# Kernel optimization log

Hardware: AMD Instinct MI355X
Metric: run time of the kernel (lower is better)

## Reference

```python
import jax
import jax.numpy as jnp
import numpy as np

B, S, I, H, O = 64, 2048, 128, 128, 128


def setup_inputs() -> dict:
    key = jax.random.key(0)
    ks = jax.random.split(key, 6)
    scale_i = 1.0 / np.sqrt(I)
    scale_h = 1.0 / np.sqrt(H)
    return {
        "x": jax.random.normal(ks[0], (B, S, I), dtype=jnp.float32),
        "Wi": jax.random.normal(ks[1], (I, H), dtype=jnp.float32) * scale_i,
        "Wh": jax.random.normal(ks[2], (H, H), dtype=jnp.float32) * scale_h,
        "b": jax.random.normal(ks[3], (H,), dtype=jnp.float32) * 0.01,
        "Wo": jax.random.normal(ks[4], (H, O), dtype=jnp.float32) * scale_h,
        "bo": jax.random.normal(ks[5], (O,), dtype=jnp.float32) * 0.01,
    }


def reference(x, Wi, Wh, b, Wo, bo):
    # x: [B, S, I]. Recurrence: h_t = relu(tanh(x_t @ Wi + h_{t-1} @ Wh + b))
    # (flax nnx.RNNCell applies tanh inside; the module applies relu on the carry.)
    h0 = jnp.zeros((x.shape[0], Wh.shape[0]), dtype=x.dtype)
    # Pre-compute input projection for all timesteps in one big GEMM.
    xi = jnp.einsum("bsi,ih->bsh", x, Wi) + b  # [B, S, H]

    def step(h, xi_t):
        h_new = jax.nn.relu(jnp.tanh(xi_t + h @ Wh))
        return h_new, h_new

    _, hs = jax.lax.scan(step, h0, jnp.swapaxes(xi, 0, 1))  # hs: [S, B, H]
    h_stacked = jnp.swapaxes(hs, 0, 1)  # [B, S, H]
    y = jnp.einsum("bsh,ho->bso", h_stacked, Wo) + bo  # [B, S, O]
    return y
```

## Files before the change

kernel.cpp:

```cpp
#include <hip/hip_runtime.h>

#define BB 64
#define SS 2048
#define HH 128

__device__ __forceinline__ void lds_barrier() {
  asm volatile("s_waitcnt lgkmcnt(0)\n\ts_barrier" ::: "memory");
}

__global__ __launch_bounds__(256) void gemm128v2(const float* __restrict__ in,
                                                 const float* __restrict__ W,
                                                 const float* __restrict__ bias,
                                                 float* __restrict__ out) {
  __shared__ __align__(16) float xls[128 * 128];
  __shared__ __align__(16) float wls[128 * 140];
  const int t = threadIdx.x;
  const long row0 = (long)blockIdx.x * 128;

  {
    const float4* g4 = (const float4*)(in + row0 * 128);
    float4* l4 = (float4*)xls;
#pragma unroll
    for (int it = 0; it < 16; ++it) l4[t + 256 * it] = g4[t + 256 * it];
  }
  {
#pragma unroll
    for (int it = 0; it < 16; ++it) {
      const int fidx = (t + 256 * it) * 4;
      const int k = fidx >> 7, j = fidx & 127;
      const float4 v = *(const float4*)(W + fidx);
      *(float4*)(wls + k * 140 + j + 4 * (j >> 5)) = v;
    }
  }
  __syncthreads();

  const int rg = t >> 4, cg = t & 15;
  const float* xrow = xls + (rg * 8) * 128;
  const float* wcol = wls + cg * 8 + 4 * (cg >> 2);

  float4 acc0[8], acc1[8];
#pragma unroll
  for (int r = 0; r < 8; ++r) {
    acc0[r] = make_float4(0.f, 0.f, 0.f, 0.f);
    acc1[r] = make_float4(0.f, 0.f, 0.f, 0.f);
  }

  for (int k = 0; k < 128; k += 4) {
    float4 xv[8];
#pragma unroll
    for (int r = 0; r < 8; ++r) xv[r] = *(const float4*)(xrow + r * 128 + k);
#pragma unroll
    for (int kk = 0; kk < 4; ++kk) {
      const float* wr = wcol + (k + kk) * 140;
      const float4 w0 = *(const float4*)(wr);
      const float4 w1 = *(const float4*)(wr + 4);
#pragma unroll
      for (int r = 0; r < 8; ++r) {
        const float xs = (kk == 0) ? xv[r].x : (kk == 1) ? xv[r].y
                       : (kk == 2) ? xv[r].z : xv[r].w;
        acc0[r].x = fmaf(xs, w0.x, acc0[r].x);
        acc0[r].y = fmaf(xs, w0.y, acc0[r].y);
        acc0[r].z = fmaf(xs, w0.z, acc0[r].z);
        acc0[r].w = fmaf(xs, w0.w, acc0[r].w);
        acc1[r].x = fmaf(xs, w1.x, acc1[r].x);
        acc1[r].y = fmaf(xs, w1.y, acc1[r].y);
        acc1[r].z = fmaf(xs, w1.z, acc1[r].z);
        acc1[r].w = fmaf(xs, w1.w, acc1[r].w);
      }
    }
  }

  const float4 b0 = *(const float4*)(bias + cg * 8);
  const float4 b1 = *(const float4*)(bias + cg * 8 + 4);
  float* op = out + (row0 + rg * 8) * 128 + cg * 8;
#pragma unroll
  for (int r = 0; r < 8; ++r) {
    float4 o0, o1;
    o0.x = acc0[r].x + b0.x; o0.y = acc0[r].y + b0.y;
    o0.z = acc0[r].z + b0.z; o0.w = acc0[r].w + b0.w;
    o1.x = acc1[r].x + b1.x; o1.y = acc1[r].y + b1.y;
    o1.z = acc1[r].z + b1.z; o1.w = acc1[r].w + b1.w;
    *(float4*)(op + r * 128) = o0;
    *(float4*)(op + r * 128 + 4) = o1;
  }
}

#define F4(s, W, A)                                                   \
  A.x = fmaf(s, W.x, A.x); A.y = fmaf(s, W.y, A.y);                   \
  A.z = fmaf(s, W.z, A.z); A.w = fmaf(s, W.w, A.w);

__global__ __attribute__((amdgpu_waves_per_eu(1, 1)))
__launch_bounds__(256) void rnn_rec4w(float* __restrict__ xi,
                                      const float* __restrict__ Wh) {
  __shared__ __align__(16) float hbuf[2][160];
  const int tid = threadIdx.x;
  const int jg = tid >> 3;
  const int kg = tid & 7;

  const int c0 = kg & 3, c1 = c0 ^ 1, c2 = c0 ^ 2, c3 = c0 ^ 3;
  const float* wbase = Wh + (kg * 16) * HH + jg * 4;
#define LDW(q) make_float4(wbase[(q) * HH + c0], wbase[(q) * HH + c1], \
                           wbase[(q) * HH + c2], wbase[(q) * HH + c3])
  const float4 W0 = LDW(0),  W1 = LDW(1),  W2 = LDW(2),  W3 = LDW(3);
  const float4 W4 = LDW(4),  W5 = LDW(5),  W6 = LDW(6),  W7 = LDW(7);
  const float4 W8 = LDW(8),  W9 = LDW(9),  W10 = LDW(10), W11 = LDW(11);
  const float4 W12 = LDW(12), W13 = LDW(13), W14 = LDW(14), W15 = LDW(15);
#undef LDW

  if (tid < 160) hbuf[0][tid] = 0.0f;

  const int col = jg * 4 + c0;
  const int hwoff = (col >> 4) * 20 + (col & 15);
  float* xb = xi + (size_t)blockIdx.x * SS * HH + col;

  constexpr int PF = 8;
  float pre[PF];
  if (kg < 4) {
#pragma unroll
    for (int p = 0; p < PF; ++p) pre[p] = xb[(size_t)p * HH];
  }
  __syncthreads();

  const float* hrd0 = hbuf[0] + kg * 20;
  const float* hrd1 = hbuf[1] + kg * 20;

  for (int t0 = 0; t0 < SS; t0 += PF) {
#pragma unroll
    for (int p = 0; p < PF; ++p) {
      const int t = t0 + p;
      const float4* h4 = (const float4*)((p & 1) ? hrd1 : hrd0);
      const float4 hv0 = h4[0], hv1 = h4[1], hv2 = h4[2], hv3 = h4[3];

      float4 a0 = make_float4(0.f, 0.f, 0.f, 0.f);
      float4 a1 = make_float4(0.f, 0.f, 0.f, 0.f);
      float4 a2 = make_float4(0.f, 0.f, 0.f, 0.f);
      float4 a3 = make_float4(0.f, 0.f, 0.f, 0.f);
      F4(hv0.x, W0, a0)  F4(hv0.y, W1, a1)  F4(hv0.z, W2, a2)  F4(hv0.w, W3, a3)
      F4(hv1.x, W4, a0)  F4(hv1.y, W5, a1)  F4(hv1.z, W6, a2)  F4(hv1.w, W7, a3)
      F4(hv2.x, W8, a0)  F4(hv2.y, W9, a1)  F4(hv2.z, W10, a2) F4(hv2.w, W11, a3)
      F4(hv3.x, W12, a0) F4(hv3.y, W13, a1) F4(hv3.z, W14, a2) F4(hv3.w, W15, a3)

      float4 pp;
      pp.x = (a0.x + a1.x) + (a2.x + a3.x);
      pp.y = (a0.y + a1.y) + (a2.y + a3.y);
      pp.z = (a0.z + a1.z) + (a2.z + a3.z);
      pp.w = (a0.w + a1.w) + (a2.w + a3.w);
      const float q0 = pp.x + __shfl_xor(pp.y, 1);
      const float q1 = pp.z + __shfl_xor(pp.w, 1);
      const float rr = q0 + __shfl_xor(q1, 2);
      const float ss = rr + __shfl_xor(rr, 4);

      if (kg < 4) {
        const float v = ss + pre[p];
        const float e = __builtin_amdgcn_exp2f(v * 2.8853900817779268f);
        const float hn =
            fmaxf(1.0f - 2.0f * __builtin_amdgcn_rcpf(e + 1.0f), 0.0f);
        hbuf[(p & 1) ^ 1][hwoff] = hn;
        xb[(size_t)t * HH] = hn;
        const int tn = t + PF;
        if (tn < SS) pre[p] = xb[(size_t)tn * HH];
      }
      lds_barrier();
    }
  }
}

extern "C" void kernel_launch(void* const* d_in, const int* in_sizes, int n_in,
                              void* d_out, int out_size, void* d_ws, size_t ws_size,
                              hipStream_t stream) {
  const float* x  = (const float*)d_in[0];
  const float* Wi = (const float*)d_in[1];
  const float* Wh = (const float*)d_in[2];
  const float* b  = (const float*)d_in[3];
  const float* Wo = (const float*)d_in[4];
  const float* bo = (const float*)d_in[5];
  float* y  = (float*)d_out;
  float* xi = (float*)d_ws;

  gemm128v2<<<(BB * SS) / 128, 256, 0, stream>>>(x, Wi, b, xi);
  rnn_rec4w<<<BB, 256, 0, stream>>>(xi, Wh);
  gemm128v2<<<(BB * SS) / 128, 256, 0, stream>>>(xi, Wo, bo, y);
}
```

Baseline: 1.001 ms.

## Repartition recurrent matvec to 4-way K split with DPP quad reductions

After: 857.7 us. 14.3% less time.

```diff
diff --git a/kernel.cpp b/kernel.cpp
--- a/kernel.cpp
+++ b/kernel.cpp
@@ -7,6 +7,10 @@
 __device__ __forceinline__ void lds_barrier() {
   asm volatile("s_waitcnt lgkmcnt(0)\n\ts_barrier" ::: "memory");
 }
+
+#define QPERM_F(x, ctrl)                                                  \
+  __int_as_float(__builtin_amdgcn_update_dpp(0, __float_as_int(x), ctrl,  \
+                                             0xF, 0xF, false))
 
 __global__ __launch_bounds__(256) void gemm128v2(const float* __restrict__ in,
                                                  const float* __restrict__ W,
@@ -85,44 +89,50 @@
   }
 }
 
-#define F4(s, W, A)                                                   \
-  A.x = fmaf(s, W.x, A.x); A.y = fmaf(s, W.y, A.y);                   \
-  A.z = fmaf(s, W.z, A.z); A.w = fmaf(s, W.w, A.w);
+#define FQ(hv, Wa, Wb, Wc, Wd)                                     \
+  a0.x = fmaf(hv.x, Wa.x, a0.x); a0.y = fmaf(hv.x, Wa.y, a0.y);    \
+  a1.x = fmaf(hv.y, Wb.x, a1.x); a1.y = fmaf(hv.y, Wb.y, a1.y);    \
+  a2.x = fmaf(hv.z, Wc.x, a2.x); a2.y = fmaf(hv.z, Wc.y, a2.y);    \
+  a3.x = fmaf(hv.w, Wd.x, a3.x); a3.y = fmaf(hv.w, Wd.y, a3.y);
 
 __global__ __attribute__((amdgpu_waves_per_eu(1, 1)))
-__launch_bounds__(256) void rnn_rec4w(float* __restrict__ xi,
-                                      const float* __restrict__ Wh) {
-  __shared__ __align__(16) float hbuf[2][160];
+__launch_bounds__(256) void rnn_dpp(float* __restrict__ xi,
+                                    const float* __restrict__ Wh) {
+  __shared__ __align__(16) float hbuf[2][144];
   const int tid = threadIdx.x;
-  const int jg = tid >> 3;
-  const int kg = tid & 7;
+  const int jg = tid >> 2;
+  const int kg = tid & 3;
+  const int j2 = jg * 2;
 
-  const int c0 = kg & 3, c1 = c0 ^ 1, c2 = c0 ^ 2, c3 = c0 ^ 3;
-  const float* wbase = Wh + (kg * 16) * HH + jg * 4;
-#define LDW(q) make_float4(wbase[(q) * HH + c0], wbase[(q) * HH + c1], \
-                           wbase[(q) * HH + c2], wbase[(q) * HH + c3])
-  const float4 W0 = LDW(0),  W1 = LDW(1),  W2 = LDW(2),  W3 = LDW(3);
-  const float4 W4 = LDW(4),  W5 = LDW(5),  W6 = LDW(6),  W7 = LDW(7);
-  const float4 W8 = LDW(8),  W9 = LDW(9),  W10 = LDW(10), W11 = LDW(11);
-  const float4 W12 = LDW(12), W13 = LDW(13), W14 = LDW(14), W15 = LDW(15);
-#undef LDW
+  const int cown = j2 + (kg & 1);
+  const int cpart = j2 + ((kg & 1) ^ 1);
+  const float* wbase = Wh + (kg * 32) * HH;
+#define LDW2(q) make_float2(wbase[(q) * HH + cown], wbase[(q) * HH + cpart])
+  const float2 W00 = LDW2(0),  W01 = LDW2(1),  W02 = LDW2(2),  W03 = LDW2(3);
+  const float2 W04 = LDW2(4),  W05 = LDW2(5),  W06 = LDW2(6),  W07 = LDW2(7);
+  const float2 W08 = LDW2(8),  W09 = LDW2(9),  W10 = LDW2(10), W11 = LDW2(11);
+  const float2 W12 = LDW2(12), W13 = LDW2(13), W14 = LDW2(14), W15 = LDW2(15);
+  const float2 W16 = LDW2(16), W17 = LDW2(17), W18 = LDW2(18), W19 = LDW2(19);
+  const float2 W20 = LDW2(20), W21 = LDW2(21), W22 = LDW2(22), W23 = LDW2(23);
+  const float2 W24 = LDW2(24), W25 = LDW2(25), W26 = LDW2(26), W27 = LDW2(27);
+  const float2 W28 = LDW2(28), W29 = LDW2(29), W30 = LDW2(30), W31 = LDW2(31);
+#undef LDW2
 
-  if (tid < 160) hbuf[0][tid] = 0.0f;
+  if (tid < 144) hbuf[0][tid] = 0.0f;
 
-  const int col = jg * 4 + c0;
-  const int hwoff = (col >> 4) * 20 + (col & 15);
-  float* xb = xi + (size_t)blockIdx.x * SS * HH + col;
+  const int hwoff = (cown >> 5) * 36 + (cown & 31);
+  float* xb = xi + (size_t)blockIdx.x * SS * HH + cown;
 
   constexpr int PF = 8;
   float pre[PF];
-  if (kg < 4) {
+  if (kg < 2) {
 #pragma unroll
     for (int p = 0; p < PF; ++p) pre[p] = xb[(size_t)p * HH];
   }
   __syncthreads();
 
-  const float* hrd0 = hbuf[0] + kg * 20;
-  const float* hrd1 = hbuf[1] + kg * 20;
+  const float* hrd0 = hbuf[0] + kg * 36;
+  const float* hrd1 = hbuf[1] + kg * 36;
 
   for (int t0 = 0; t0 < SS; t0 += PF) {
 #pragma unroll
@@ -130,28 +140,26 @@
       const int t = t0 + p;
       const float4* h4 = (const float4*)((p & 1) ? hrd1 : hrd0);
       const float4 hv0 = h4[0], hv1 = h4[1], hv2 = h4[2], hv3 = h4[3];
+      const float4 hv4 = h4[4], hv5 = h4[5], hv6 = h4[6], hv7 = h4[7];
 
-      float4 a0 = make_float4(0.f, 0.f, 0.f, 0.f);
-      float4 a1 = make_float4(0.f, 0.f, 0.f, 0.f);
-      float4 a2 = make_float4(0.f, 0.f, 0.f, 0.f);
-      float4 a3 = make_float4(0.f, 0.f, 0.f, 0.f);
-      F4(hv0.x, W0, a0)  F4(hv0.y, W1, a1)  F4(hv0.z, W2, a2)  F4(hv0.w, W3, a3)
-      F4(hv1.x, W4, a0)  F4(hv1.y, W5, a1)  F4(hv1.z, W6, a2)  F4(hv1.w, W7, a3)
-      F4(hv2.x, W8, a0)  F4(hv2.y, W9, a1)  F4(hv2.z, W10, a2) F4(hv2.w, W11, a3)
-      F4(hv3.x, W12, a0) F4(hv3.y, W13, a1) F4(hv3.z, W14, a2) F4(hv3.w, W15, a3)
+      float2 a0 = make_float2(0.f, 0.f), a1 = make_float2(0.f, 0.f);
+      float2 a2 = make_float2(0.f, 0.f), a3 = make_float2(0.f, 0.f);
+      FQ(hv0, W00, W01, W02, W03)
+      FQ(hv1, W04, W05, W06, W07)
+      FQ(hv2, W08, W09, W10, W11)
+      FQ(hv3, W12, W13, W14, W15)
+      FQ(hv4, W16, W17, W18, W19)
+      FQ(hv5, W20, W21, W22, W23)
+      FQ(hv6, W24, W25, W26, W27)
+      FQ(hv7, W28, W29, W30, W31)
 
-      float4 pp;
-      pp.x = (a0.x + a1.x) + (a2.x + a3.x);
-      pp.y = (a0.y + a1.y) + (a2.y + a3.y);
-      pp.z = (a0.z + a1.z) + (a2.z + a3.z);
-      pp.w = (a0.w + a1.w) + (a2.w + a3.w);
-      const float q0 = pp.x + __shfl_xor(pp.y, 1);
-      const float q1 = pp.z + __shfl_xor(pp.w, 1);
-      const float rr = q0 + __shfl_xor(q1, 2);
-      const float ss = rr + __shfl_xor(rr, 4);
+      const float px = (a0.x + a1.x) + (a2.x + a3.x);
+      const float py = (a0.y + a1.y) + (a2.y + a3.y);
+      const float q0 = px + QPERM_F(py, 0xB1);
+      const float s = q0 + QPERM_F(q0, 0x4E);
 
-      if (kg < 4) {
-        const float v = ss + pre[p];
+      if (kg < 2) {
+        const float v = s + pre[p];
         const float e = __builtin_amdgcn_exp2f(v * 2.8853900817779268f);
         const float hn =
             fmaxf(1.0f - 2.0f * __builtin_amdgcn_rcpf(e + 1.0f), 0.0f);
@@ -178,6 +186,6 @@
   float* xi = (float*)d_ws;
 
   gemm128v2<<<(BB * SS) / 128, 256, 0, stream>>>(x, Wi, b, xi);
-  rnn_rec4w<<<BB, 256, 0, stream>>>(xi, Wh);
+  rnn_dpp<<<BB, 256, 0, stream>>>(xi, Wh);
   gemm128v2<<<(BB * SS) / 128, 256, 0, stream>>>(xi, Wo, bo, y);
 }
```

## Rework RNN recurrence thread mapping to use DPP and permlane swaps for reduction

Applied to the files above, without the earlier changes.

Measured after the change: 850.0 us. -15.0%, faster.

```diff
diff --git a/kernel.cpp b/kernel.cpp
--- a/kernel.cpp
+++ b/kernel.cpp
@@ -7,6 +7,10 @@
 __device__ __forceinline__ void lds_barrier() {
   asm volatile("s_waitcnt lgkmcnt(0)\n\ts_barrier" ::: "memory");
 }
+
+#define QPERM_F(x, ctrl)                                                  \
+  __int_as_float(__builtin_amdgcn_update_dpp(0, __float_as_int(x), ctrl,  \
+                                             0xF, 0xF, false))
 
 __global__ __launch_bounds__(256) void gemm128v2(const float* __restrict__ in,
                                                  const float* __restrict__ W,
@@ -85,77 +89,92 @@
   }
 }
 
-#define F4(s, W, A)                                                   \
-  A.x = fmaf(s, W.x, A.x); A.y = fmaf(s, W.y, A.y);                   \
-  A.z = fmaf(s, W.z, A.z); A.w = fmaf(s, W.w, A.w);
+#define FK(hk, WA, WB)                                                 \
+  pA.x = fmaf(hk, WA.x, pA.x); pA.y = fmaf(hk, WA.y, pA.y);            \
+  pA.z = fmaf(hk, WA.z, pA.z); pA.w = fmaf(hk, WA.w, pA.w);            \
+  pB.x = fmaf(hk, WB.x, pB.x); pB.y = fmaf(hk, WB.y, pB.y);            \
+  pB.z = fmaf(hk, WB.z, pB.z); pB.w = fmaf(hk, WB.w, pB.w);
 
 __global__ __attribute__((amdgpu_waves_per_eu(1, 1)))
-__launch_bounds__(256) void rnn_rec4w(float* __restrict__ xi,
+__launch_bounds__(256) void rnn_dpp16(float* __restrict__ xi,
                                       const float* __restrict__ Wh) {
-  __shared__ __align__(16) float hbuf[2][160];
+  __shared__ __align__(16) float hbuf[2][192];
   const int tid = threadIdx.x;
-  const int jg = tid >> 3;
-  const int kg = tid & 7;
-
-  const int c0 = kg & 3, c1 = c0 ^ 1, c2 = c0 ^ 2, c3 = c0 ^ 3;
-  const float* wbase = Wh + (kg * 16) * HH + jg * 4;
-#define LDW(q) make_float4(wbase[(q) * HH + c0], wbase[(q) * HH + c1], \
-                           wbase[(q) * HH + c2], wbase[(q) * HH + c3])
-  const float4 W0 = LDW(0),  W1 = LDW(1),  W2 = LDW(2),  W3 = LDW(3);
-  const float4 W4 = LDW(4),  W5 = LDW(5),  W6 = LDW(6),  W7 = LDW(7);
-  const float4 W8 = LDW(8),  W9 = LDW(9),  W10 = LDW(10), W11 = LDW(11);
-  const float4 W12 = LDW(12), W13 = LDW(13), W14 = LDW(14), W15 = LDW(15);
-#undef LDW
-
-  if (tid < 160) hbuf[0][tid] = 0.0f;
-
-  const int col = jg * 4 + c0;
-  const int hwoff = (col >> 4) * 20 + (col & 15);
+  const int l = tid & 63;
+  const int w = tid >> 6;
+  const int f = (l & 3) | (((l >> 4) & 1) << 2);
+  const int K = f | (((l >> 5) & 1) << 3);
+  const int jg = ((l >> 2) & 3) | (w << 2);
+  const bool own = ((l >> 5) & 1) == 0;
+  const int col = jg * 8 + f;
+
+  const float* wb_ = Wh + (K * 8) * HH + jg * 8;
+#define LW(k)                                                              \
+  const float4 W##k##A = make_float4(wb_[(k) * HH + (0 ^ f)],              \
+                                     wb_[(k) * HH + (1 ^ f)],              \
+                                     wb_[(k) * HH + (2 ^ f)],              \
+                                     wb_[(k) * HH + (3 ^ f)]);             \
+  const float4 W##k##B = make_float4(wb_[(k) * HH + (4 ^ f)],              \
+                                     wb_[(k) * HH + (5 ^ f)],              \
+                                     wb_[(k) * HH + (6 ^ f)],              \
+                                     wb_[(k) * HH + (7 ^ f)]);
+  LW(0) LW(1) LW(2) LW(3) LW(4) LW(5) LW(6) LW(7)
+#undef LW
+
+  if (tid < 192) hbuf[0][tid] = 0.0f;
+
+  const int rdoff = K * 12;
+  const int wroff = (col >> 3) * 12 + (col & 7);
   float* xb = xi + (size_t)blockIdx.x * SS * HH + col;
 
   constexpr int PF = 8;
   float pre[PF];
-  if (kg < 4) {
+#pragma unroll
+  for (int p = 0; p < PF; ++p) pre[p] = 0.0f;
+  if (own) {
 #pragma unroll
     for (int p = 0; p < PF; ++p) pre[p] = xb[(size_t)p * HH];
   }
   __syncthreads();
-
-  const float* hrd0 = hbuf[0] + kg * 20;
-  const float* hrd1 = hbuf[1] + kg * 20;
 
   for (int t0 = 0; t0 < SS; t0 += PF) {
 #pragma unroll
     for (int p = 0; p < PF; ++p) {
       const int t = t0 + p;
-      const float4* h4 = (const float4*)((p & 1) ? hrd1 : hrd0);
-      const float4 hv0 = h4[0], hv1 = h4[1], hv2 = h4[2], hv3 = h4[3];
-
-      float4 a0 = make_float4(0.f, 0.f, 0.f, 0.f);
-      float4 a1 = make_float4(0.f, 0.f, 0.f, 0.f);
-      float4 a2 = make_float4(0.f, 0.f, 0.f, 0.f);
-      float4 a3 = make_float4(0.f, 0.f, 0.f, 0.f);
-      F4(hv0.x, W0, a0)  F4(hv0.y, W1, a1)  F4(hv0.z, W2, a2)  F4(hv0.w, W3, a3)
-      F4(hv1.x, W4, a0)  F4(hv1.y, W5, a1)  F4(hv1.z, W6, a2)  F4(hv1.w, W7, a3)
-      F4(hv2.x, W8, a0)  F4(hv2.y, W9, a1)  F4(hv2.z, W10, a2) F4(hv2.w, W11, a3)
-      F4(hv3.x, W12, a0) F4(hv3.y, W13, a1) F4(hv3.z, W14, a2) F4(hv3.w, W15, a3)
-
-      float4 pp;
-      pp.x = (a0.x + a1.x) + (a2.x + a3.x);
-      pp.y = (a0.y + a1.y) + (a2.y + a3.y);
-      pp.z = (a0.z + a1.z) + (a2.z + a3.z);
-      pp.w = (a0.w + a1.w) + (a2.w + a3.w);
-      const float q0 = pp.x + __shfl_xor(pp.y, 1);
-      const float q1 = pp.z + __shfl_xor(pp.w, 1);
-      const float rr = q0 + __shfl_xor(q1, 2);
-      const float ss = rr + __shfl_xor(rr, 4);
-
-      if (kg < 4) {
-        const float v = ss + pre[p];
-        const float e = __builtin_amdgcn_exp2f(v * 2.8853900817779268f);
-        const float hn =
-            fmaxf(1.0f - 2.0f * __builtin_amdgcn_rcpf(e + 1.0f), 0.0f);
-        hbuf[(p & 1) ^ 1][hwoff] = hn;
+      const float* hb = hbuf[p & 1] + rdoff;
+      const float4 h0 = *(const float4*)(hb);
+      const float4 h1 = *(const float4*)(hb + 4);
+
+      float4 pA = make_float4(0.f, 0.f, 0.f, 0.f);
+      float4 pB = make_float4(0.f, 0.f, 0.f, 0.f);
+      FK(h0.x, W0A, W0B) FK(h0.y, W1A, W1B)
+      FK(h0.z, W2A, W2B) FK(h0.w, W3A, W3B)
+      FK(h1.x, W4A, W4B) FK(h1.y, W5A, W5B)
+      FK(h1.z, W6A, W6B) FK(h1.w, W7A, W7B)
+
+      const float q0 = pA.x + QPERM_F(pA.y, 0xB1);
+      const float q1 = pA.z + QPERM_F(pA.w, 0xB1);
+      const float q2 = pB.x + QPERM_F(pB.y, 0xB1);
+      const float q3 = pB.z + QPERM_F(pB.w, 0xB1);
+      const float r0 = q0 + QPERM_F(q1, 0x4E);
+      const float r1 = q2 + QPERM_F(q3, 0x4E);
+      int va = __float_as_int(r1), vb;
+      asm volatile("v_mov_b32 %1, %0\n\ts_nop 1\n\tv_permlane16_swap_b32 %0, %1"
+                   : "+v"(va), "=&v"(vb));
+      const float tt =
+          r0 + ((__int_as_float(va) + __int_as_float(vb)) - r1);
+      int wa = __float_as_int(tt), wbv;
+      asm volatile("v_mov_b32 %1, %0\n\ts_nop 1\n\tv_permlane32_swap_b32 %0, %1"
+                   : "+v"(wa), "=&v"(wbv));
+      const float sfin = __int_as_float(wa) + __int_as_float(wbv);
+
+      const float v = sfin + pre[p];
+      const float e = __builtin_amdgcn_exp2f(v * 2.8853900817779268f);
+      const float hn =
+          fmaxf(1.0f - 2.0f * __builtin_amdgcn_rcpf(e + 1.0f), 0.0f);
+
+      if (own) {
+        hbuf[(p & 1) ^ 1][wroff] = hn;
         xb[(size_t)t * HH] = hn;
         const int tn = t + PF;
         if (tn < SS) pre[p] = xb[(size_t)tn * HH];
@@ -178,6 +197,6 @@
   float* xi = (float*)d_ws;
 
   gemm128v2<<<(BB * SS) / 128, 256, 0, stream>>>(x, Wi, b, xi);
-  rnn_rec4w<<<BB, 256, 0, stream>>>(xi, Wh);
+  rnn_dpp16<<<BB, 256, 0, stream>>>(xi, Wh);
   gemm128v2<<<(BB * SS) / 128, 256, 0, stream>>>(xi, Wo, bo, y);
 }
```
